# Kernel tuning notes

Measured on AMD Instinct MI355X. Metric: run time of the kernel, lower is better.

Reference implementation:

```python
import jax, jax.numpy as jnp
import numpy as np


def _dF(field, c):
    """Central differences of component c of field [B,X,Y,Z,C] -> [B,X-2,Y-2,Z-2,3]."""
    f = field[..., c]
    dx = (f[:, 2:, 1:-1, 1:-1] - f[:, :-2, 1:-1, 1:-1]) * 0.5
    dy = (f[:, 1:-1, 2:, 1:-1] - f[:, 1:-1, :-2, 1:-1]) * 0.5
    dz = (f[:, 1:-1, 1:-1, 2:] - f[:, 1:-1, 1:-1, :-2]) * 0.5
    return jnp.stack((dx, dy, dz), axis=4)


def setup_inputs() -> dict:
    key = jax.random.key(0)
    grid = jax.random.normal(key, (2, 160, 160, 160, 3), dtype=jnp.float32)
    return {"grid": grid}


def reference(grid):
    # First derivatives of each displacement component: [B,X-2,Y-2,Z-2,3]
    dx = _dF(grid, 0)
    dy = _dF(grid, 1)
    dz = _dF(grid, 2)
    # Second derivatives: [B,X-4,Y-4,Z-4,3]
    dxx = _dF(dx, 0)
    dyy = _dF(dy, 1)
    dzz = _dF(dz, 2)
    dxy = _dF(dx, 1)
    dyz = _dF(dy, 2)
    dxz = _dF(dx, 2)
    penalty = jnp.sum(dxx ** 2 + dyy ** 2 + dzz ** 2
                      + 2.0 * (dxy ** 2 + dyz ** 2 + dxz ** 2))
    return penalty / dxx.size
```

## Files before the change

### kernel.cpp

```cpp
#include <hip/hip_runtime.h>

#define OY 480
#define OX 76800
#define SB 12288000
#define JT 12
#define KT 39
#define IT 39
#define NBLK 416
#define ROWF 129
#define RW 132
#define NROW 16
#define SLICE (NROW*RW)
#define NBUF 6
#define SLICE_FLOATS (NROW*ROWF)
#define PTS (JT*KT)
#define INV_SIZE (1.0f/22778496.0f)

__global__ __launch_bounds__(512)
void be_partials(const float* __restrict__ g, float* __restrict__ partial) {
    __shared__ float lds[NBUF * SLICE];
    __shared__ float wsum[8];

    const int tid = threadIdx.x;
    const int bid = blockIdx.x;
    const int kt  = bid & 3;
    const int is  = (bid >> 2) & 3;
    const int r   = bid >> 4;
    const int jt  = r % 13;
    const int bb  = r / 13;

    const int j0  = jt * JT;
    const int k0z = kt * KT;
    const int ib  = is * IT;

    const float* __restrict__ G = g + (size_t)bb * SB;

    int gd0, gd1, gd2, gd3, gd4 = 0, ld0, ld1, ld2, ld3, ld4 = 0;
    {
        int f, row, pos;
        f = tid;        row = f / ROWF; pos = f - row * ROWF;
        gd0 = (j0 + row) * OY + k0z * 3 + pos;  ld0 = row * RW + pos;
        f = tid + 512;  row = f / ROWF; pos = f - row * ROWF;
        gd1 = (j0 + row) * OY + k0z * 3 + pos;  ld1 = row * RW + pos;
        f = tid + 1024; row = f / ROWF; pos = f - row * ROWF;
        gd2 = (j0 + row) * OY + k0z * 3 + pos;  ld2 = row * RW + pos;
        f = tid + 1536; row = f / ROWF; pos = f - row * ROWF;
        gd3 = (j0 + row) * OY + k0z * 3 + pos;  ld3 = row * RW + pos;
    }
    const bool tail = (tid < SLICE_FLOATS - 2048);
    if (tail) {
        int f = tid + 2048; int row = f / ROWF; int pos = f - row * ROWF;
        gd4 = (j0 + row) * OY + k0z * 3 + pos;  ld4 = row * RW + pos;
    }

    const bool act = tid < PTS;
    int jj = tid / KT;
    int kk = tid - jj * KT;
    if (!act) { jj = 0; kk = 0; }
    const int cbase = (jj + 2) * RW + (kk + 2) * 3;

    #pragma unroll
    for (int w = 0; w < 5; ++w) {
        const int x = ib + w;
        const float* base = G + (size_t)x * OX;
        float a0 = base[gd0], a1 = base[gd1], a2 = base[gd2], a3 = base[gd3];
        float a4 = tail ? base[gd4] : 0.0f;
        float* L = lds + (x % NBUF) * SLICE;
        L[ld0] = a0; L[ld1] = a1; L[ld2] = a2; L[ld3] = a3;
        if (tail) L[ld4] = a4;
    }
    __syncthreads();

    float s = 0.0f;
    for (int i0 = ib; i0 < ib + IT; ++i0) {
        const int xn = i0 + 5;
        const bool doLoad = (xn <= ib + 42);
        float a0 = 0.f, a1 = 0.f, a2 = 0.f, a3 = 0.f, a4 = 0.f;
        if (doLoad) {
            const float* base = G + (size_t)xn * OX;
            a0 = base[gd0]; a1 = base[gd1]; a2 = base[gd2]; a3 = base[gd3];
            if (tail) a4 = base[gd4];
        }

        if (act) {
            int s0 = i0 % NBUF;
            int s1 = s0 + 1; if (s1 >= NBUF) s1 -= NBUF;
            int s2 = s1 + 1; if (s2 >= NBUF) s2 -= NBUF;
            int s3 = s2 + 1; if (s3 >= NBUF) s3 -= NBUF;
            int s4 = s3 + 1; if (s4 >= NBUF) s4 -= NBUF;
            const float* Sm2 = lds + s0 * SLICE + cbase;
            const float* Sm1 = lds + s1 * SLICE + cbase;
            const float* Sc  = lds + s2 * SLICE + cbase;
            const float* Sp1 = lds + s3 * SLICE + cbase;
            const float* Sp2 = lds + s4 * SLICE + cbase;

            const float c0 = Sc[0], c1 = Sc[1], c2 = Sc[2];
            float hzz0 = Sc[6] - 2.0f*c0 + Sc[-6];
            float hzz1 = Sc[7] - 2.0f*c1 + Sc[-5];
            float hzz2 = Sc[8] - 2.0f*c2 + Sc[-4];
            float hyy0 = Sc[ 2*RW]     - 2.0f*c0 + Sc[-2*RW];
            float hyy1 = Sc[ 2*RW + 1] - 2.0f*c1 + Sc[-2*RW + 1];
            float hxx0 = Sp2[0] - 2.0f*c0 + Sm2[0];
            float hyz0 = (Sc[RW+3] - Sc[RW-3]) - (Sc[-RW+3] - Sc[-RW-3]);
            float hyz1 = (Sc[RW+4] - Sc[RW-2]) - (Sc[-RW+4] - Sc[-RW-2]);
            float hyz2 = (Sc[RW+5] - Sc[RW-1]) - (Sc[-RW+5] - Sc[-RW-1]);
            float hxy0 = (Sp1[ RW]   - Sp1[-RW])   - (Sm1[ RW]   - Sm1[-RW]);
            float hxy1 = (Sp1[ RW+1] - Sp1[-RW+1]) - (Sm1[ RW+1] - Sm1[-RW+1]);
            float hxz0 = (Sp1[3] - Sp1[-3]) - (Sm1[3] - Sm1[-3]);
            float hxz1 = (Sp1[4] - Sp1[-2]) - (Sm1[4] - Sm1[-2]);
            float hxz2 = (Sp1[5] - Sp1[-1]) - (Sm1[5] - Sm1[-1]);

            float w1 = hxx0*hxx0;
            w1 = fmaf(hyy1, hyy1, w1); w1 = fmaf(hzz2, hzz2, w1);
            w1 = fmaf(hxy1, hxy1, w1); w1 = fmaf(hxz2, hxz2, w1);
            w1 = fmaf(hyz2, hyz2, w1);
            float w2 = hyy0*hyy0;
            w2 = fmaf(hzz0, hzz0, w2); w2 = fmaf(hzz1, hzz1, w2);
            w2 = fmaf(hxz1, hxz1, w2);
            float w3 = hxy0*hxy0;
            w3 = fmaf(hxz0, hxz0, w3); w3 = fmaf(hyz1, hyz1, w3);
            float w4 = hyz0*hyz0;

            float t = fmaf(2.0f, w2, w1);
            t = fmaf(3.0f, w3, t);
            t = fmaf(4.0f, w4, t);
            s = fmaf(0.0625f, t, s);
        }

        if (doLoad) {
            float* L = lds + (xn % NBUF) * SLICE;
            L[ld0] = a0; L[ld1] = a1; L[ld2] = a2; L[ld3] = a3;
            if (tail) L[ld4] = a4;
        }
        __syncthreads();
    }

    #pragma unroll
    for (int off = 32; off > 0; off >>= 1) s += __shfl_down(s, off, 64);
    if ((tid & 63) == 0) wsum[tid >> 6] = s;
    __syncthreads();
    if (tid == 0) {
        float tot = 0.0f;
        #pragma unroll
        for (int w = 0; w < 8; ++w) tot += wsum[w];
        partial[bid] = tot;
    }
}

__global__ __launch_bounds__(256)
void be_final(const float* __restrict__ partial, float* __restrict__ out) {
    float s = 0.0f;
    for (int i = threadIdx.x; i < NBLK; i += 256) s += partial[i];
    #pragma unroll
    for (int off = 32; off > 0; off >>= 1) s += __shfl_down(s, off, 64);
    __shared__ float ws[4];
    if ((threadIdx.x & 63) == 0) ws[threadIdx.x >> 6] = s;
    __syncthreads();
    if (threadIdx.x == 0)
        out[0] = ((ws[0] + ws[1]) + (ws[2] + ws[3])) * INV_SIZE;
}

extern "C" void kernel_launch(void* const* d_in, const int* in_sizes, int n_in,
                              void* d_out, int out_size, void* d_ws, size_t ws_size,
                              hipStream_t stream) {
    const float* grid = (const float*)d_in[0];
    float* out = (float*)d_out;
    float* partials = (float*)d_ws;

    be_partials<<<dim3(NBLK), dim3(512), 0, stream>>>(grid, partials);
    be_final<<<1, 256, 0, stream>>>(partials, out);
}
```

Before: 169.7 us.

## Compute four z-points per thread with vectorized LDS and global float4 loads

Each compute thread now covers four consecutive z-points (12 floats), using wide float4/float2 loads from shared memory so neighbouring stencil values are shared in registers. Global-to-LDS staging moves to float4 accesses with a wider padded row. Block shape changes to 256 threads with 52-wide z tiles and 26-slice x chunks, which raises block count and halo overhead along x. The aim is to cut LDS instruction count and global load count per output point, at the cost of higher register pressure and fewer active compute threads per block.

```diff
diff --git a/kernel.cpp b/kernel.cpp
--- a/kernel.cpp
+++ b/kernel.cpp
@@ -4,133 +4,187 @@
 #define OX 76800
 #define SB 12288000
 #define JT 12
-#define KT 39
-#define IT 39
-#define NBLK 416
-#define ROWF 129
-#define RW 132
+#define KT 52
+#define IT 26
+#define NBLK 468
+#define RWF 168
 #define NROW 16
-#define SLICE (NROW*RW)
+#define SLICE (NROW*RWF)
 #define NBUF 6
-#define SLICE_FLOATS (NROW*ROWF)
-#define PTS (JT*KT)
+#define NF4 (SLICE/4)
+#define NSTR 13
+#define CTHR (JT*NSTR)
 #define INV_SIZE (1.0f/22778496.0f)
 
-__global__ __launch_bounds__(512)
+__device__ __forceinline__ void ld24(float* d, const float* s) {
+    #pragma unroll
+    for (int q = 0; q < 6; ++q)
+        *(float4*)(d + 4*q) = *(const float4*)(s + 4*q);
+}
+__device__ __forceinline__ void ld12(float* d, const float* s) {
+    *(float2*)(d)      = *(const float2*)(s);
+    *(float4*)(d + 2)  = *(const float4*)(s + 2);
+    *(float4*)(d + 6)  = *(const float4*)(s + 6);
+    *(float2*)(d + 10) = *(const float2*)(s + 10);
+}
+
+__global__ __launch_bounds__(256, 2)
 void be_partials(const float* __restrict__ g, float* __restrict__ partial) {
     __shared__ float lds[NBUF * SLICE];
-    __shared__ float wsum[8];
+    __shared__ float wsum[4];
 
     const int tid = threadIdx.x;
     const int bid = blockIdx.x;
-    const int kt  = bid & 3;
-    const int is  = (bid >> 2) & 3;
-    const int r   = bid >> 4;
-    const int jt  = r % 13;
-    const int bb  = r / 13;
-
-    const int j0  = jt * JT;
-    const int k0z = kt * KT;
-    const int ib  = is * IT;
+    const int is  = bid % 6;
+    const int r1  = bid / 6;
+    const int kt  = r1 % 3;
+    const int r2  = r1 / 3;
+    const int jt  = r2 % 13;
+    const int bb  = r2 / 13;
+
+    const int i_start = is * IT;
+    const int j0      = jt * JT;
+    const int k0f     = kt * 156;
 
     const float* __restrict__ G = g + (size_t)bb * SB;
 
-    int gd0, gd1, gd2, gd3, gd4 = 0, ld0, ld1, ld2, ld3, ld4 = 0;
+    int gfl0, gfl1, gfl2 = 0, lfl0, lfl1, lfl2 = 0;
     {
-        int f, row, pos;
-        f = tid;        row = f / ROWF; pos = f - row * ROWF;
-        gd0 = (j0 + row) * OY + k0z * 3 + pos;  ld0 = row * RW + pos;
-        f = tid + 512;  row = f / ROWF; pos = f - row * ROWF;
-        gd1 = (j0 + row) * OY + k0z * 3 + pos;  ld1 = row * RW + pos;
-        f = tid + 1024; row = f / ROWF; pos = f - row * ROWF;
-        gd2 = (j0 + row) * OY + k0z * 3 + pos;  ld2 = row * RW + pos;
-        f = tid + 1536; row = f / ROWF; pos = f - row * ROWF;
-        gd3 = (j0 + row) * OY + k0z * 3 + pos;  ld3 = row * RW + pos;
-    }
-    const bool tail = (tid < SLICE_FLOATS - 2048);
+        int f4, row, pos;
+        f4 = tid;        row = f4 / 42; pos = f4 - row * 42;
+        gfl0 = (j0 + row) * OY + k0f + 4 * pos;  lfl0 = row * RWF + 4 * pos;
+        f4 = tid + 256;  row = f4 / 42; pos = f4 - row * 42;
+        gfl1 = (j0 + row) * OY + k0f + 4 * pos;  lfl1 = row * RWF + 4 * pos;
+    }
+    const bool tail = tid < (NF4 - 512);
     if (tail) {
-        int f = tid + 2048; int row = f / ROWF; int pos = f - row * ROWF;
-        gd4 = (j0 + row) * OY + k0z * 3 + pos;  ld4 = row * RW + pos;
-    }
-
-    const bool act = tid < PTS;
-    int jj = tid / KT;
-    int kk = tid - jj * KT;
-    if (!act) { jj = 0; kk = 0; }
-    const int cbase = (jj + 2) * RW + (kk + 2) * 3;
+        int f4 = tid + 512; int row = f4 / 42; int pos = f4 - row * 42;
+        gfl2 = (j0 + row) * OY + k0f + 4 * pos;  lfl2 = row * RWF + 4 * pos;
+    }
+
+    const bool act = tid < CTHR;
+    int jj = tid / NSTR;
+    int ss = tid - jj * NSTR;
+    if (!act) { jj = 0; ss = 0; }
+    const int rb = (jj + 2) * RWF + 12 * ss;
 
     #pragma unroll
     for (int w = 0; w < 5; ++w) {
-        const int x = ib + w;
-        const float* base = G + (size_t)x * OX;
-        float a0 = base[gd0], a1 = base[gd1], a2 = base[gd2], a3 = base[gd3];
-        float a4 = tail ? base[gd4] : 0.0f;
-        float* L = lds + (x % NBUF) * SLICE;
-        L[ld0] = a0; L[ld1] = a1; L[ld2] = a2; L[ld3] = a3;
-        if (tail) L[ld4] = a4;
+        const int gx = i_start + w;
+        const float* base = G + (size_t)gx * OX;
+        float4 v0 = *(const float4*)(base + gfl0);
+        float4 v1 = *(const float4*)(base + gfl1);
+        float4 v2 = tail ? *(const float4*)(base + gfl2) : make_float4(0,0,0,0);
+        float* L = lds + (gx % NBUF) * SLICE;
+        *(float4*)(L + lfl0) = v0;
+        *(float4*)(L + lfl1) = v1;
+        if (tail) *(float4*)(L + lfl2) = v2;
     }
     __syncthreads();
 
     float s = 0.0f;
-    for (int i0 = ib; i0 < ib + IT; ++i0) {
-        const int xn = i0 + 5;
-        const bool doLoad = (xn <= ib + 42);
-        float a0 = 0.f, a1 = 0.f, a2 = 0.f, a3 = 0.f, a4 = 0.f;
+    for (int i0 = 0; i0 < IT; ++i0) {
+        const int gx = i_start + i0;
+
+        const bool doLoad = (i0 < IT - 1);
+        float4 v0 = make_float4(0,0,0,0), v1 = v0, v2 = v0;
         if (doLoad) {
-            const float* base = G + (size_t)xn * OX;
-            a0 = base[gd0]; a1 = base[gd1]; a2 = base[gd2]; a3 = base[gd3];
-            if (tail) a4 = base[gd4];
+            const float* base = G + (size_t)(gx + 5) * OX;
+            v0 = *(const float4*)(base + gfl0);
+            v1 = *(const float4*)(base + gfl1);
+            if (tail) v2 = *(const float4*)(base + gfl2);
         }
 
         if (act) {
-            int s0 = i0 % NBUF;
-            int s1 = s0 + 1; if (s1 >= NBUF) s1 -= NBUF;
-            int s2 = s1 + 1; if (s2 >= NBUF) s2 -= NBUF;
-            int s3 = s2 + 1; if (s3 >= NBUF) s3 -= NBUF;
-            int s4 = s3 + 1; if (s4 >= NBUF) s4 -= NBUF;
-            const float* Sm2 = lds + s0 * SLICE + cbase;
-            const float* Sm1 = lds + s1 * SLICE + cbase;
-            const float* Sc  = lds + s2 * SLICE + cbase;
-            const float* Sp1 = lds + s3 * SLICE + cbase;
-            const float* Sp2 = lds + s4 * SLICE + cbase;
-
-            const float c0 = Sc[0], c1 = Sc[1], c2 = Sc[2];
-            float hzz0 = Sc[6] - 2.0f*c0 + Sc[-6];
-            float hzz1 = Sc[7] - 2.0f*c1 + Sc[-5];
-            float hzz2 = Sc[8] - 2.0f*c2 + Sc[-4];
-            float hyy0 = Sc[ 2*RW]     - 2.0f*c0 + Sc[-2*RW];
-            float hyy1 = Sc[ 2*RW + 1] - 2.0f*c1 + Sc[-2*RW + 1];
-            float hxx0 = Sp2[0] - 2.0f*c0 + Sm2[0];
-            float hyz0 = (Sc[RW+3] - Sc[RW-3]) - (Sc[-RW+3] - Sc[-RW-3]);
-            float hyz1 = (Sc[RW+4] - Sc[RW-2]) - (Sc[-RW+4] - Sc[-RW-2]);
-            float hyz2 = (Sc[RW+5] - Sc[RW-1]) - (Sc[-RW+5] - Sc[-RW-1]);
-            float hxy0 = (Sp1[ RW]   - Sp1[-RW])   - (Sm1[ RW]   - Sm1[-RW]);
-            float hxy1 = (Sp1[ RW+1] - Sp1[-RW+1]) - (Sm1[ RW+1] - Sm1[-RW+1]);
-            float hxz0 = (Sp1[3] - Sp1[-3]) - (Sm1[3] - Sm1[-3]);
-            float hxz1 = (Sp1[4] - Sp1[-2]) - (Sm1[4] - Sm1[-2]);
-            float hxz2 = (Sp1[5] - Sp1[-1]) - (Sm1[5] - Sm1[-1]);
-
-            float w1 = hxx0*hxx0;
-            w1 = fmaf(hyy1, hyy1, w1); w1 = fmaf(hzz2, hzz2, w1);
-            w1 = fmaf(hxy1, hxy1, w1); w1 = fmaf(hxz2, hxz2, w1);
-            w1 = fmaf(hyz2, hyz2, w1);
-            float w2 = hyy0*hyy0;
-            w2 = fmaf(hzz0, hzz0, w2); w2 = fmaf(hzz1, hzz1, w2);
-            w2 = fmaf(hxz1, hxz1, w2);
-            float w3 = hxy0*hxy0;
-            w3 = fmaf(hxz0, hxz0, w3); w3 = fmaf(hyz1, hyz1, w3);
-            float w4 = hyz0*hyz0;
-
-            float t = fmaf(2.0f, w2, w1);
-            t = fmaf(3.0f, w3, t);
-            t = fmaf(4.0f, w4, t);
+            const float* S0 = lds + ((gx    ) % NBUF) * SLICE;
+            const float* S1 = lds + ((gx + 1) % NBUF) * SLICE;
+            const float* S2 = lds + ((gx + 2) % NBUF) * SLICE;
+            const float* S3 = lds + ((gx + 3) % NBUF) * SLICE;
+            const float* S4 = lds + ((gx + 4) % NBUF) * SLICE;
+
+            float w1a = 0.f, w2a = 0.f, w3a = 0.f, w4a = 0.f;
+
+            float C[24]; ld24(C, S2 + rb);
+
+            {
+                float U[12], D[12];
+                ld12(U, S2 + rb + 2*RWF + 6);
+                ld12(D, S2 + rb - 2*RWF + 6);
+                #pragma unroll
+                for (int p = 0; p < 4; ++p) {
+                    float hyy0 = U[3*p]   - 2.0f*C[6+3*p]   + D[3*p];
+                    float hyy1 = U[3*p+1] - 2.0f*C[6+3*p+1] + D[3*p+1];
+                    w2a = fmaf(hyy0, hyy0, w2a);
+                    w1a = fmaf(hyy1, hyy1, w1a);
+                }
+            }
+            {
+                float A[24], Bv[24];
+                ld24(A,  S2 + rb + RWF);
+                ld24(Bv, S2 + rb - RWF);
+                #pragma unroll
+                for (int p = 0; p < 4; ++p) {
+                    const int o = 3 * p;
+                    float hzz0 = C[12+o]   - 2.0f*C[6+o]   + C[o];
+                    float hzz1 = C[12+o+1] - 2.0f*C[6+o+1] + C[o+1];
+                    float hzz2 = C[12+o+2] - 2.0f*C[6+o+2] + C[o+2];
+                    w2a = fmaf(hzz0, hzz0, w2a);
+                    w2a = fmaf(hzz1, hzz1, w2a);
+                    w1a = fmaf(hzz2, hzz2, w1a);
+                    float hyz0 = (A[9+o]   - A[3+o])   - (Bv[9+o]   - Bv[3+o]);
+                    float hyz1 = (A[9+o+1] - A[3+o+1]) - (Bv[9+o+1] - Bv[3+o+1]);
+                    float hyz2 = (A[9+o+2] - A[3+o+2]) - (Bv[9+o+2] - Bv[3+o+2]);
+                    w4a = fmaf(hyz0, hyz0, w4a);
+                    w3a = fmaf(hyz1, hyz1, w3a);
+                    w1a = fmaf(hyz2, hyz2, w1a);
+                }
+            }
+            {
+                float P[24], M[24];
+                ld24(P, S3 + rb);
+                ld24(M, S1 + rb);
+                #pragma unroll
+                for (int p = 0; p < 4; ++p) {
+                    const int o = 3 * p;
+                    float hxz0 = (P[9+o]   - P[3+o])   - (M[9+o]   - M[3+o]);
+                    float hxz1 = (P[9+o+1] - P[3+o+1]) - (M[9+o+1] - M[3+o+1]);
+                    float hxz2 = (P[9+o+2] - P[3+o+2]) - (M[9+o+2] - M[3+o+2]);
+                    w3a = fmaf(hxz0, hxz0, w3a);
+                    w2a = fmaf(hxz1, hxz1, w2a);
+                    w1a = fmaf(hxz2, hxz2, w1a);
+                }
+            }
+            {
+                float PU[12], PD[12], MU[12], MD[12];
+                ld12(PU, S3 + rb + RWF + 6);
+                ld12(PD, S3 + rb - RWF + 6);
+                ld12(MU, S1 + rb + RWF + 6);
+                ld12(MD, S1 + rb - RWF + 6);
+                #pragma unroll
+                for (int p = 0; p < 4; ++p) {
+                    float hxy0 = (PU[3*p]   - PD[3*p])   - (MU[3*p]   - MD[3*p]);
+                    float hxy1 = (PU[3*p+1] - PD[3*p+1]) - (MU[3*p+1] - MD[3*p+1]);
+                    w3a = fmaf(hxy0, hxy0, w3a);
+                    w1a = fmaf(hxy1, hxy1, w1a);
+                }
+            }
+            #pragma unroll
+            for (int p = 0; p < 4; ++p) {
+                float hxx0 = S4[rb + 6 + 3*p] - 2.0f*C[6+3*p] + S0[rb + 6 + 3*p];
+                w1a = fmaf(hxx0, hxx0, w1a);
+            }
+
+            float t = fmaf(2.0f, w2a, w1a);
+            t = fmaf(3.0f, w3a, t);
+            t = fmaf(4.0f, w4a, t);
             s = fmaf(0.0625f, t, s);
         }
 
         if (doLoad) {
-            float* L = lds + (xn % NBUF) * SLICE;
-            L[ld0] = a0; L[ld1] = a1; L[ld2] = a2; L[ld3] = a3;
-            if (tail) L[ld4] = a4;
+            float* L = lds + ((gx + 5) % NBUF) * SLICE;
+            *(float4*)(L + lfl0) = v0;
+            *(float4*)(L + lfl1) = v1;
+            if (tail) *(float4*)(L + lfl2) = v2;
         }
         __syncthreads();
     }
@@ -139,12 +193,8 @@
     for (int off = 32; off > 0; off >>= 1) s += __shfl_down(s, off, 64);
     if ((tid & 63) == 0) wsum[tid >> 6] = s;
     __syncthreads();
-    if (tid == 0) {
-        float tot = 0.0f;
-        #pragma unroll
-        for (int w = 0; w < 8; ++w) tot += wsum[w];
-        partial[bid] = tot;
-    }
+    if (tid == 0)
+        partial[bid] = (wsum[0] + wsum[1]) + (wsum[2] + wsum[3]);
 }
 
 __global__ __launch_bounds__(256)
@@ -167,6 +217,6 @@
     float* out = (float*)d_out;
     float* partials = (float*)d_ws;
 
-    be_partials<<<dim3(NBLK), dim3(512), 0, stream>>>(grid, partials);
+    be_partials<<<dim3(NBLK), dim3(256), 0, stream>>>(grid, partials);
     be_final<<<1, 256, 0, stream>>>(partials, out);
 }
```

New measurement: 191.6 us. +12.9%, slower.
